# Performance work log

Measured on AMD Instinct MI355X. Metric: run time of the kernel, lower is better.

## Reference

```python
import jax, jax.numpy as jnp
import numpy as np

IMG_W, IMG_H = 640, 480
OS = 8            # roialign output_size
SCALE = 1.0       # spatial_scale (boxes already mapped to feature coords)
ALIGNED = True
ALPHA = 1.0       # student-t alpha


def _roi_align_one(feat, boxes):
    # feat: [C, H, W]; boxes: [sn, 4] (x1, y1, x2, y2) in feature coords.
    # torchvision RoIAlign, sampling_ratio=1 (one sample at each bin center).
    C, H, W = feat.shape
    off = 0.5 if ALIGNED else 0.0
    x1 = boxes[:, 0] * SCALE - off
    y1 = boxes[:, 1] * SCALE - off
    x2 = boxes[:, 2] * SCALE - off
    y2 = boxes[:, 3] * SCALE - off
    bw = (x2 - x1) / OS   # bin width  [sn]
    bh = (y2 - y1) / OS   # bin height [sn]
    grid = jnp.arange(OS, dtype=feat.dtype) + 0.5
    xs = x1[:, None] + grid * bw[:, None]   # [sn, OS]
    ys = y1[:, None] + grid * bh[:, None]   # [sn, OS]
    X = jnp.broadcast_to(xs[:, None, :], (xs.shape[0], OS, OS))  # [sn,OS,OS]
    Y = jnp.broadcast_to(ys[:, :, None], (ys.shape[0], OS, OS))
    valid = (Y >= -1.0) & (Y <= H) & (X >= -1.0) & (X <= W)
    y = jnp.clip(Y, 0.0, H - 1)
    x = jnp.clip(X, 0.0, W - 1)
    y0f = jnp.floor(y); x0f = jnp.floor(x)
    y0 = y0f.astype(jnp.int32); x0 = x0f.astype(jnp.int32)
    y1i = jnp.minimum(y0 + 1, H - 1); x1i = jnp.minimum(x0 + 1, W - 1)
    ly = y - y0f; lx = x - x0f
    hy = 1.0 - ly; hx = 1.0 - lx
    def g(yi, xi):
        return feat[:, yi, xi]  # [C, sn, OS, OS]
    val = (hy * hx)[None] * g(y0, x0) + (hy * lx)[None] * g(y0, x1i) \
        + (ly * hx)[None] * g(y1i, x0) + (ly * lx)[None] * g(y1i, x1i)
    val = jnp.where(valid[None], val, 0.0)
    return jnp.transpose(val, (1, 0, 2, 3))  # [sn, C, OS, OS]


def setup_inputs() -> dict:
    key = jax.random.key(0)
    ks = jax.random.split(key, 10)
    B, SN, C, T, FY, FX = 16, 64, 480, 2, 60, 80
    NDF1, NDF2, K = 1024, 256, 64
    z = jax.random.normal(ks[0], (B, C, T, FY, FX), jnp.float32)
    # boxes in image pixel coords
    cx = jax.random.uniform(ks[1], (B, SN), minval=0.1, maxval=0.9) * IMG_W
    cy = jax.random.uniform(ks[2], (B, SN), minval=0.1, maxval=0.9) * IMG_H
    bw = jax.random.uniform(ks[3], (B, SN), minval=0.05, maxval=0.3) * IMG_W
    bh = jax.random.uniform(ks[4], (B, SN), minval=0.05, maxval=0.3) * IMG_H
    x1 = jnp.clip(cx - bw / 2, 0.0, IMG_W); x2 = jnp.clip(cx + bw / 2, 0.0, IMG_W)
    y1 = jnp.clip(cy - bh / 2, 0.0, IMG_H); y2 = jnp.clip(cy + bh / 2, 0.0, IMG_H)
    bboxs = jnp.stack([x1, y1, x2, y2], axis=-1).astype(jnp.float32)
    din = C * OS * OS
    w1 = jax.random.normal(ks[5], (NDF1, din), jnp.float32) * (din ** -0.5)
    b1 = jnp.zeros((NDF1,), jnp.float32)
    w2 = jax.random.normal(ks[6], (NDF2, NDF1), jnp.float32) * (NDF1 ** -0.5)
    b2 = jnp.zeros((NDF2,), jnp.float32)
    centroids = jax.random.normal(ks[7], (K, NDF2), jnp.float32)
    return {"z": z, "bboxs": bboxs, "w1": w1, "b1": b1, "w2": w2, "b2": b2,
            "centroids": centroids}


def reference(z, bboxs, w1, b1, w2, b2, centroids):
    B, C, T, fy, fx = z.shape
    sn = bboxs.shape[1]
    # scale image-space boxes to feature coords (per (x,y) pair as in torch code)
    sc = jnp.array([fx / IMG_W, fy / IMG_H], jnp.float32)
    bb = (bboxs.reshape(B, sn, 2, 2) * sc).reshape(B, sn, 4)
    bb = jnp.nan_to_num(bb)
    feat = z[:, :, -1]  # [B, C, fy, fx]
    pooled = jax.vmap(_roi_align_one)(feat, bb)  # [B, sn, C, OS, OS]
    flat = pooled.reshape(B * sn, -1)
    e = flat @ w1.T + b1
    e = e @ w2.T + b2
    zz = e.reshape(B, sn, -1)  # [B, sn, ndf2]
    # student-t soft assignment (faithful: L2 norm, not squared)
    z2 = jnp.sum(zz * zz, axis=-1, keepdims=True)          # [B,sn,1]
    c2 = jnp.sum(centroids * centroids, axis=-1)           # [K]
    zc = jnp.einsum('bsd,kd->bsk', zz, centroids)          # [B,sn,K]
    nrm = jnp.sqrt(jnp.maximum(z2 + c2 - 2.0 * zc, 0.0))
    s = ((1.0 + nrm) / ALPHA) ** (-(ALPHA + 1.0) / 2.0)
    s = s / jnp.sum(s, axis=-1, keepdims=True)
    c = jnp.argmax(s, axis=2)
    return zz, s, c
```

## Files before the change

### kernel.cpp

```cpp
#include <hip/hip_runtime.h>
#include <hip/hip_bf16.h>

static constexpr int B_  = 16;
static constexpr int SN_ = 64;
static constexpr int C_  = 480;
static constexpr int T_  = 2;
static constexpr int FY_ = 60;
static constexpr int FX_ = 80;
static constexpr int OS_ = 8;
static constexpr int DIN = 30720;
static constexpr int M_  = 1024;
static constexpr int N1_ = 1024;
static constexpr int N2_ = 256;
static constexpr int K_  = 64;
static constexpr int SPLITK = 16;
static constexpr int NCH_ZZ = (DIN / 64) / SPLITK;
static constexpr int NCH_FW = N1_ / 32;
static constexpr int CPB = 2;
static constexpr int IMG = FY_ * FX_;
static constexpr int NB_W1T = (DIN / 64) * (N1_ / 64);
static constexpr int NB_W2P = N2_;
static constexpr int NB_FW  = 480;
static constexpr int NB_ROI = 16 * (C_ / CPB);

typedef __bf16 bf16x8 __attribute__((ext_vector_type(8)));
typedef float  f32x4  __attribute__((ext_vector_type(4)));
typedef unsigned int u32_as1 __attribute__((address_space(1)));
typedef unsigned int u32_as3 __attribute__((address_space(3)));

__device__ __forceinline__ float bf2f(unsigned short u) {
    union { unsigned int i; float f; } v; v.i = ((unsigned int)u) << 16; return v.f;
}
__device__ __forceinline__ unsigned short f2bf(float f) {
    unsigned int u = __float_as_uint(f);
    u = u + 0x7FFFu + ((u >> 16) & 1u);
    return (unsigned short)(u >> 16);
}
__device__ __forceinline__ void gll16(const void* g, void* l) {
    __builtin_amdgcn_global_load_lds((const u32_as1*)g, (u32_as3*)l, 16, 0, 0);
}

template<int NCHUNK, int SEG>
__device__ __forceinline__ void gemm_core(
    const unsigned short* __restrict__ Abase, long long Astride,
    const unsigned short* __restrict__ Bbase, long long Bstride,
    int k0, f32x4 (&acc)[4][2], unsigned short* L)
{
    const int t = threadIdx.x;
    const int w = t >> 6, lane = t & 63;
    const int rl8 = lane >> 3, slot = lane & 7;
    const int wm = w >> 2, wn = w & 3;
    const int fr = lane & 15, fg = lane >> 4;
    const int swz8 = (slot ^ rl8) * 8;

    long long arow[2], brow[2];
    int ci[2];
#pragma unroll
    for (int c = 0; c < 2; ++c) {
        ci[c] = w * 2 + c;
        const int row = ci[c] * 8 + rl8;
        arow[c] = (long long)row * Astride;
        brow[c] = (long long)row * Bstride;
    }

    auto stage = [&](int chunk, int par) {
        const int kin = k0 + chunk * 64;
        char* Lp = (char*)L + par * 65536;
#pragma unroll
        for (int c = 0; c < 2; ++c) {
            gll16(Abase + arow[c] + kin + swz8,       Lp + 0 * 16384 + ci[c] * 1024);
            gll16(Abase + arow[c] + SEG + kin + swz8, Lp + 1 * 16384 + ci[c] * 1024);
            gll16(Bbase + brow[c] + kin + swz8,       Lp + 2 * 16384 + ci[c] * 1024);
            gll16(Bbase + brow[c] + SEG + kin + swz8, Lp + 3 * 16384 + ci[c] * 1024);
        }
    };

    stage(0, 0);
    stage(1, 1);

    for (int it = 0; it < NCHUNK; ++it) {
        const int par = it & 1;
        if (it + 1 < NCHUNK) asm volatile("s_waitcnt vmcnt(8)" ::: "memory");
        else                 asm volatile("s_waitcnt vmcnt(0)" ::: "memory");
        __builtin_amdgcn_s_barrier();

        const char* Lp = (const char*)L + par * 65536;
        bf16x8 a[2][2][4], b[2][2][2];
#pragma unroll
        for (int hl = 0; hl < 2; ++hl)
#pragma unroll
            for (int ks = 0; ks < 2; ++ks)
#pragma unroll
                for (int mf = 0; mf < 4; ++mf) {
                    const int row = wm * 64 + mf * 16 + fr;
                    a[hl][ks][mf] = *reinterpret_cast<const bf16x8*>(
                        Lp + hl * 16384 + row * 128 + 16 * ((ks * 4 + fg) ^ (fr & 7)));
                }
#pragma unroll
        for (int hl = 0; hl < 2; ++hl)
#pragma unroll
            for (int ks = 0; ks < 2; ++ks)
#pragma unroll
                for (int nf = 0; nf < 2; ++nf) {
                    const int row = wn * 32 + nf * 16 + fr;
                    b[hl][ks][nf] = *reinterpret_cast<const bf16x8*>(
                        Lp + (2 + hl) * 16384 + row * 128 + 16 * ((ks * 4 + fg) ^ (fr & 7)));
                }
        asm volatile("s_waitcnt lgkmcnt(0)" ::: "memory");
        __builtin_amdgcn_sched_barrier(0);
        __builtin_amdgcn_s_barrier();
        __builtin_amdgcn_sched_barrier(0);
        if (it + 2 < NCHUNK) stage(it + 2, par);
        __builtin_amdgcn_sched_barrier(0);

        __builtin_amdgcn_s_setprio(1);
#pragma unroll
        for (int ks = 0; ks < 2; ++ks)
#pragma unroll
            for (int mf = 0; mf < 4; ++mf)
#pragma unroll
                for (int nf = 0; nf < 2; ++nf) {
                    acc[mf][nf] = __builtin_amdgcn_mfma_f32_16x16x32_bf16(
                        a[0][ks][mf], b[0][ks][nf], acc[mf][nf], 0, 0, 0);
                    acc[mf][nf] = __builtin_amdgcn_mfma_f32_16x16x32_bf16(
                        a[0][ks][mf], b[1][ks][nf], acc[mf][nf], 0, 0, 0);
                    acc[mf][nf] = __builtin_amdgcn_mfma_f32_16x16x32_bf16(
                        a[1][ks][mf], b[0][ks][nf], acc[mf][nf], 0, 0, 0);
                }
        __builtin_amdgcn_s_setprio(0);
    }
}

template<int NCHUNK, int SEG>
__device__ __forceinline__ void gemm_core32(
    const unsigned short* __restrict__ Abase, long long Astride,
    const unsigned short* __restrict__ Bbase, long long Bstride,
    int k0, f32x4 (&acc)[4][2], unsigned short* L)
{
    const int t = threadIdx.x;
    const int w = t >> 6, lane = t & 63;
    const int rl8 = lane >> 3, slot = lane & 7;
    const int wm = w >> 2, wn = w & 3;
    const int fr = lane & 15, fg = lane >> 4;
    const int g    = slot ^ rl8;
    const int goff = (g < 4) ? g * 8 : SEG + (g - 4) * 8;

    long long arow[2], brow[2];
    int ci[2];
#pragma unroll
    for (int c = 0; c < 2; ++c) {
        ci[c] = w * 2 + c;
        const int row = ci[c] * 8 + rl8;
        arow[c] = (long long)row * Astride;
        brow[c] = (long long)row * Bstride;
    }

    auto stage = [&](int chunk, int par) {
        const int kin = k0 + chunk * 32;
        char* Lp = (char*)L + par * 32768;
#pragma unroll
        for (int c = 0; c < 2; ++c) {
            gll16(Abase + arow[c] + goff + kin, Lp + 0 * 16384 + ci[c] * 1024);
            gll16(Bbase + brow[c] + goff + kin, Lp + 1 * 16384 + ci[c] * 1024);
        }
    };

    stage(0, 0);
    stage(1, 1);

    for (int it = 0; it < NCHUNK; ++it) {
        const int par = it & 1;
        if (it + 1 < NCHUNK) asm volatile("s_waitcnt vmcnt(4)" ::: "memory");
        else                 asm volatile("s_waitcnt vmcnt(0)" ::: "memory");
        __builtin_amdgcn_s_barrier();

        const char* Lp = (const char*)L + par * 32768;
        bf16x8 a[2][4], b[2][2];
#pragma unroll
        for (int hl = 0; hl < 2; ++hl)
#pragma unroll
            for (int mf = 0; mf < 4; ++mf) {
                const int row = wm * 64 + mf * 16 + fr;
                a[hl][mf] = *reinterpret_cast<const bf16x8*>(
                    Lp + row * 128 + 16 * ((hl * 4 + fg) ^ (fr & 7)));
            }
#pragma unroll
        for (int hl = 0; hl < 2; ++hl)
#pragma unroll
            for (int nf = 0; nf < 2; ++nf) {
                const int row = wn * 32 + nf * 16 + fr;
                b[hl][nf] = *reinterpret_cast<const bf16x8*>(
                    Lp + 16384 + row * 128 + 16 * ((hl * 4 + fg) ^ (fr & 7)));
            }
        asm volatile("s_waitcnt lgkmcnt(0)" ::: "memory");
        __builtin_amdgcn_sched_barrier(0);
        __builtin_amdgcn_s_barrier();
        __builtin_amdgcn_sched_barrier(0);
        if (it + 2 < NCHUNK) stage(it + 2, par);
        __builtin_amdgcn_sched_barrier(0);

        __builtin_amdgcn_s_setprio(1);
#pragma unroll
        for (int mf = 0; mf < 4; ++mf)
#pragma unroll
            for (int nf = 0; nf < 2; ++nf) {
                acc[mf][nf] = __builtin_amdgcn_mfma_f32_16x16x32_bf16(
                    a[0][mf], b[0][nf], acc[mf][nf], 0, 0, 0);
                acc[mf][nf] = __builtin_amdgcn_mfma_f32_16x16x32_bf16(
                    a[0][mf], b[1][nf], acc[mf][nf], 0, 0, 0);
                acc[mf][nf] = __builtin_amdgcn_mfma_f32_16x16x32_bf16(
                    a[1][mf], b[0][nf], acc[mf][nf], 0, 0, 0);
            }
        __builtin_amdgcn_s_setprio(0);
    }
}

__global__ __launch_bounds__(256) void prep1_kernel(
    const float* __restrict__ w1, const float* __restrict__ w2,
    const float* __restrict__ b1, const float* __restrict__ b2,
    unsigned short* __restrict__ w1T2, unsigned short* __restrict__ w2cat,
    float* __restrict__ bf) {
    __shared__ __align__(16) char smem[16640];
    const int blk = blockIdx.x;
    const int t = threadIdx.x;

    if (blk < NB_W1T) {
        float (*L)[65] = (float (*)[65])smem;
        const int q0 = (blk % (DIN / 64)) * 64, j0 = (blk / (DIN / 64)) * 64;
        const int tr = t >> 4, tc4 = (t & 15) * 4;
#pragma unroll
        for (int jj = 0; jj < 4; ++jj) {
            const int j = jj * 16 + tr;
            const float4 v = *(const float4*)(w1 + (size_t)(j0 + j) * DIN + q0 + tc4);
            L[j][tc4] = v.x; L[j][tc4 + 1] = v.y; L[j][tc4 + 2] = v.z; L[j][tc4 + 3] = v.w;
        }
        __syncthreads();
#pragma unroll
        for (int pass = 0; pass < 4; ++pass) {
            const int ql = pass * 16 + tr;
            const int jc = tc4;
            ushort4 h4, l4;
            float v0 = L[jc + 0][ql], v1 = L[jc + 1][ql], v2 = L[jc + 2][ql], v3 = L[jc + 3][ql];
            h4.x = f2bf(v0); l4.x = f2bf(v0 - bf2f(h4.x));
            h4.y = f2bf(v1); l4.y = f2bf(v1 - bf2f(h4.y));
            h4.z = f2bf(v2); l4.z = f2bf(v2 - bf2f(h4.z));
            h4.w = f2bf(v3); l4.w = f2bf(v3 - bf2f(h4.w));
            *(ushort4*)(w1T2 + (size_t)(q0 + ql) * 2048 + j0 + jc)        = h4;
            *(ushort4*)(w1T2 + (size_t)(q0 + ql) * 2048 + 1024 + j0 + jc) = l4;
        }
    } else {
        float* red = (float*)smem;
        const int p = blk - NB_W1T;
        float acc = 0.f;
#pragma unroll
        for (int j = t; j < N1_; j += 256) {
            const float v = w2[(size_t)p * N1_ + j];
            const unsigned short hi = f2bf(v);
            const unsigned short lo = f2bf(v - bf2f(hi));
            w2cat[(size_t)p * 2048 + j]        = hi;
            w2cat[(size_t)p * 2048 + 1024 + j] = lo;
            acc = fmaf(v, b1[j], acc);
        }
        red[t] = acc; __syncthreads();
        for (int s = 128; s > 0; s >>= 1) { if (t < s) red[t] += red[t + s]; __syncthreads(); }
        if (t == 0) bf[p] = red[0] + b2[p];
    }
}

__global__ __launch_bounds__(512, 4) void mega2_kernel(
    const float* __restrict__ z, const float* __restrict__ bboxs,
    const unsigned short* __restrict__ w2cat, const unsigned short* __restrict__ w1T2,
    unsigned short* __restrict__ W2, unsigned short* __restrict__ flat2) {
    __shared__ __align__(16) char smem[65536];
    const int blk = blockIdx.x;
    const int t = threadIdx.x;

    if (blk < NB_FW) {
        unsigned short* L = (unsigned short*)smem;
        const int xcd = blk & 7, j = blk >> 3;
        const int pb = j & 1;
        const int qb = xcd * 30 + (j >> 1);
        f32x4 acc[4][2];
#pragma unroll
        for (int i = 0; i < 4; ++i)
#pragma unroll
            for (int k = 0; k < 2; ++k) acc[i][k] = (f32x4){0.f, 0.f, 0.f, 0.f};

        gemm_core32<NCH_FW, N1_>(w2cat + (long long)pb * 128 * 2048, 2048,
                                 w1T2 + (long long)qb * 128 * 2048, 2048,
                                 0, acc, L);

        const int w = t >> 6, lane = t & 63;
        const int wm = w >> 2, wn = w & 3;
        const int fr = lane & 15, fg = lane >> 4;
#pragma unroll
        for (int mf = 0; mf < 4; ++mf)
#pragma unroll
            for (int nf = 0; nf < 2; ++nf)
#pragma unroll
                for (int r = 0; r < 4; ++r) {
                    const int p = pb * 128 + wm * 64 + mf * 16 + fg * 4 + r;
                    const int q = qb * 128 + wn * 32 + nf * 16 + fr;
                    const float v = acc[mf][nf][r];
                    const unsigned short hi = f2bf(v);
                    const unsigned short lo = f2bf(v - bf2f(hi));
                    W2[(size_t)p * (2 * DIN) + q]       = hi;
                    W2[(size_t)p * (2 * DIN) + DIN + q] = lo;
                }
    } else {
        float* img = (float*)smem;
        float (*bxc)[4] = (float (*)[4])(smem + 38400);
        const int idx = blk - NB_FW;
        const int b  = idx / (C_ / CPB);
        const int cg = idx % (C_ / CPB);
        const float* zb = z + ((size_t)b * C_ + (size_t)cg * CPB) * (size_t)(T_ * IMG)
                            + (size_t)(T_ - 1) * IMG;
#pragma unroll
        for (int c = 0; c < CPB; ++c) {
            const float4* src = (const float4*)(zb + (size_t)c * (T_ * IMG));
            float4* dst = (float4*)(img + c * IMG);
            for (int i = t; i < IMG / 4; i += 512) dst[i] = src[i];
        }
        if (t < 64) {
            const float* bp = bboxs + ((size_t)b * 64 + t) * 4;
            const float v0 = bp[0], v1 = bp[1], v2 = bp[2], v3 = bp[3];
            bxc[t][0] = isnan(v0) ? 0.f : v0;
            bxc[t][1] = isnan(v1) ? 0.f : v1;
            bxc[t][2] = isnan(v2) ? 0.f : v2;
            bxc[t][3] = isnan(v3) ? 0.f : v3;
        }
        __syncthreads();

        const int p = t & 63, mh = t >> 6;
        const int gy = p >> 3, gx = p & 7;
        for (int mq = 0; mq < 8; ++mq) {
            const int m = mq * 8 + mh;
            const float x1 = bxc[m][0] * 0.125f - 0.5f;
            const float y1 = bxc[m][1] * 0.125f - 0.5f;
            const float x2 = bxc[m][2] * 0.125f - 0.5f;
            const float y2 = bxc[m][3] * 0.125f - 0.5f;
            const float bw = (x2 - x1) * (1.0f / OS_);
            const float bh = (y2 - y1) * (1.0f / OS_);
            const float X = x1 + ((float)gx + 0.5f) * bw;
            const float Y = y1 + ((float)gy + 0.5f) * bh;
            const bool valid = (Y >= -1.0f) && (Y <= (float)FY_) &&
                               (X >= -1.0f) && (X <= (float)FX_);
            const float yc = fminf(fmaxf(Y, 0.f), (float)(FY_ - 1));
            const float xc = fminf(fmaxf(X, 0.f), (float)(FX_ - 1));
            const float y0f = floorf(yc), x0f = floorf(xc);
            const int y0 = (int)y0f, x0 = (int)x0f;
            const int y1i = min(y0 + 1, FY_ - 1);
            const int x1i = min(x0 + 1, FX_ - 1);
            const float ly = yc - y0f, lx = xc - x0f;
            const float hy = 1.f - ly,  hx = 1.f - lx;
            float w00 = hy * hx, w01 = hy * lx, w10 = ly * hx, w11 = ly * lx;
            if (!valid) { w00 = 0.f; w01 = 0.f; w10 = 0.f; w11 = 0.f; }
            const int i00 = y0 * FX_ + x0, i01 = y0 * FX_ + x1i;
            const int i10 = y1i * FX_ + x0, i11 = y1i * FX_ + x1i;
            unsigned short* fo = flat2 + (size_t)(b * 64 + m) * (2 * DIN)
                                       + cg * (CPB * 64) + p;
#pragma unroll
            for (int c = 0; c < CPB; ++c) {
                const float* f = img + c * IMG;
                const float v = w00 * f[i00] + w01 * f[i01] + w10 * f[i10] + w11 * f[i11];
                const unsigned short hi = f2bf(v);
                const unsigned short lo = f2bf(v - bf2f(hi));
                fo[c * 64]       = hi;
                fo[DIN + c * 64] = lo;
            }
        }
    }
}

__global__ __launch_bounds__(512, 1) void zz_mfma(const unsigned short* __restrict__ flat2,
                                                  const unsigned short* __restrict__ W2,
                                                  float* __restrict__ part) {
    __shared__ __align__(16) unsigned short L[2 * 4 * 128 * 64];
    const int bid = blockIdx.x;
    const int xcd = bid & 7, j = bid >> 3;
    const int mb = j & 7;
    const int pair = xcd * 4 + (j >> 3);
    const int nb = pair & 1, sp = pair >> 1;
    f32x4 acc[4][2];
#pragma unroll
    for (int i = 0; i < 4; ++i)
#pragma unroll
        for (int k = 0; k < 2; ++k) acc[i][k] = (f32x4){0.f, 0.f, 0.f, 0.f};

    gemm_core<NCH_ZZ, DIN>(flat2 + (long long)mb * 128 * (2 * DIN), 2 * DIN,
                           W2 + (long long)nb * 128 * (2 * DIN), 2 * DIN,
                           sp * (NCH_ZZ * 64), acc, L);

    float* po = part + (size_t)sp * (M_ * N2_);
    const int t = threadIdx.x;
    const int w = t >> 6, lane = t & 63;
    const int wm = w >> 2, wn = w & 3;
    const int fr = lane & 15, fg = lane >> 4;
#pragma unroll
    for (int mf = 0; mf < 4; ++mf)
#pragma unroll
        for (int nf = 0; nf < 2; ++nf)
#pragma unroll
            for (int r = 0; r < 4; ++r) {
                const int m = mb * 128 + wm * 64 + mf * 16 + fg * 4 + r;
                const int n = nb * 128 + wn * 32 + nf * 16 + fr;
                po[(size_t)m * N2_ + n] = acc[mf][nf][r];
            }
}

__global__ __launch_bounds__(256) void reduce_cluster_kernel(
    const float* __restrict__ part, const float* __restrict__ bf,
    const float* __restrict__ cent,
    float* __restrict__ out_zz, float* __restrict__ out_s, float* __restrict__ out_c) {
    __shared__ float row[N2_];
    const int m = blockIdx.x, t = threadIdx.x;
    float a = bf[t];
#pragma unroll
    for (int s = 0; s < SPLITK; ++s) a += part[(size_t)s * (M_ * N2_) + (size_t)m * N2_ + t];
    out_zz[(size_t)m * N2_ + t] = a;
    row[t] = a;
    __syncthreads();
    if (t < 64) {
        const float* cr = cent + (size_t)t * N2_;
        float dot = 0.f, c2 = 0.f, z2 = 0.f;
        for (int d = 0; d < N2_; ++d) {
            const float zv = row[d], cv = cr[d];
            dot = fmaf(zv, cv, dot);
            c2  = fmaf(cv, cv, c2);
            z2  = fmaf(zv, zv, z2);
        }
        const float nrm = sqrtf(fmaxf(z2 + c2 - 2.f * dot, 0.f));
        const float su = 1.0f / (1.0f + nrm);
        float ssum = su;
#pragma unroll
        for (int mk = 1; mk < 64; mk <<= 1) ssum += __shfl_xor(ssum, mk, 64);
        const float s = su / ssum;
        out_s[(size_t)m * 64 + t] = s;
        float bv = s; int bi = t;
#pragma unroll
        for (int mk = 1; mk < 64; mk <<= 1) {
            const float ov = __shfl_xor(bv, mk, 64);
            const int   oi = __shfl_xor(bi, mk, 64);
            if (ov > bv || (ov == bv && oi < bi)) { bv = ov; bi = oi; }
        }
        if (t == 0) out_c[m] = (float)bi;
    }
}

extern "C" void kernel_launch(void* const* d_in, const int* in_sizes, int n_in,
                              void* d_out, int out_size, void* d_ws, size_t ws_size,
                              hipStream_t stream) {
    const float* z     = (const float*)d_in[0];
    const float* bboxs = (const float*)d_in[1];
    const float* w1    = (const float*)d_in[2];
    const float* b1    = (const float*)d_in[3];
    const float* w2    = (const float*)d_in[4];
    const float* b2    = (const float*)d_in[5];
    const float* cent  = (const float*)d_in[6];
    float* out = (float*)d_out;
    float* out_zz = out;
    float* out_s  = out + (size_t)M_ * N2_;
    float* out_c  = out + (size_t)M_ * N2_ + (size_t)M_ * K_;

    char* ws = (char*)d_ws;
    unsigned short* w1T2   = (unsigned short*)(ws);
    unsigned short* flat2  = (unsigned short*)(ws + 125829120u);
    unsigned short* W2     = (unsigned short*)(ws + 251658240u);
    float*          part   = (float*)(ws + 283115520u);
    unsigned short* w2cat  = (unsigned short*)(ws + 316669952u);
    float*          bfused = (float*)(ws + 317718528u);

    prep1_kernel<<<dim3(NB_W1T + NB_W2P), dim3(256), 0, stream>>>(
        w1, w2, b1, b2, w1T2, w2cat, bfused);
    mega2_kernel<<<dim3(NB_FW + NB_ROI), dim3(512), 0, stream>>>(
        z, bboxs, w2cat, w1T2, W2, flat2);
    zz_mfma<<<dim3(256), dim3(512), 0, stream>>>(flat2, W2, part);
    reduce_cluster_kernel<<<dim3(1024), dim3(256), 0, stream>>>(part, bfused, cent,
                                                                out_zz, out_s, out_c);
}
```

Before: 228.4 us.

## Move RoIAlign pooling into prep kernel and give weight-fusion GEMM its own kernel

```diff
diff --git a/kernel.cpp b/kernel.cpp
--- a/kernel.cpp
+++ b/kernel.cpp
@@ -18,10 +18,9 @@
 static constexpr int NCH_FW = N1_ / 32;
 static constexpr int CPB = 2;
 static constexpr int IMG = FY_ * FX_;
+static constexpr int NB_ROI = 16 * (C_ / CPB);
 static constexpr int NB_W1T = (DIN / 64) * (N1_ / 64);
 static constexpr int NB_W2P = N2_;
-static constexpr int NB_FW  = 480;
-static constexpr int NB_ROI = 16 * (C_ / CPB);
 
 typedef __bf16 bf16x8 __attribute__((ext_vector_type(8)));
 typedef float  f32x4  __attribute__((ext_vector_type(4)));
@@ -215,111 +214,28 @@
     }
 }
 
-__global__ __launch_bounds__(256) void prep1_kernel(
+__global__ __launch_bounds__(256) void prep_kernel(
+    const float* __restrict__ z, const float* __restrict__ bboxs,
     const float* __restrict__ w1, const float* __restrict__ w2,
     const float* __restrict__ b1, const float* __restrict__ b2,
-    unsigned short* __restrict__ w1T2, unsigned short* __restrict__ w2cat,
-    float* __restrict__ bf) {
-    __shared__ __align__(16) char smem[16640];
+    unsigned short* __restrict__ flat2, unsigned short* __restrict__ w1T2,
+    unsigned short* __restrict__ w2cat, float* __restrict__ bf) {
+    __shared__ __align__(16) char smem[39424];
     const int blk = blockIdx.x;
     const int t = threadIdx.x;
 
-    if (blk < NB_W1T) {
-        float (*L)[65] = (float (*)[65])smem;
-        const int q0 = (blk % (DIN / 64)) * 64, j0 = (blk / (DIN / 64)) * 64;
-        const int tr = t >> 4, tc4 = (t & 15) * 4;
-#pragma unroll
-        for (int jj = 0; jj < 4; ++jj) {
-            const int j = jj * 16 + tr;
-            const float4 v = *(const float4*)(w1 + (size_t)(j0 + j) * DIN + q0 + tc4);
-            L[j][tc4] = v.x; L[j][tc4 + 1] = v.y; L[j][tc4 + 2] = v.z; L[j][tc4 + 3] = v.w;
-        }
-        __syncthreads();
-#pragma unroll
-        for (int pass = 0; pass < 4; ++pass) {
-            const int ql = pass * 16 + tr;
-            const int jc = tc4;
-            ushort4 h4, l4;
-            float v0 = L[jc + 0][ql], v1 = L[jc + 1][ql], v2 = L[jc + 2][ql], v3 = L[jc + 3][ql];
-            h4.x = f2bf(v0); l4.x = f2bf(v0 - bf2f(h4.x));
-            h4.y = f2bf(v1); l4.y = f2bf(v1 - bf2f(h4.y));
-            h4.z = f2bf(v2); l4.z = f2bf(v2 - bf2f(h4.z));
-            h4.w = f2bf(v3); l4.w = f2bf(v3 - bf2f(h4.w));
-            *(ushort4*)(w1T2 + (size_t)(q0 + ql) * 2048 + j0 + jc)        = h4;
-            *(ushort4*)(w1T2 + (size_t)(q0 + ql) * 2048 + 1024 + j0 + jc) = l4;
-        }
-    } else {
-        float* red = (float*)smem;
-        const int p = blk - NB_W1T;
-        float acc = 0.f;
-#pragma unroll
-        for (int j = t; j < N1_; j += 256) {
-            const float v = w2[(size_t)p * N1_ + j];
-            const unsigned short hi = f2bf(v);
-            const unsigned short lo = f2bf(v - bf2f(hi));
-            w2cat[(size_t)p * 2048 + j]        = hi;
-            w2cat[(size_t)p * 2048 + 1024 + j] = lo;
-            acc = fmaf(v, b1[j], acc);
-        }
-        red[t] = acc; __syncthreads();
-        for (int s = 128; s > 0; s >>= 1) { if (t < s) red[t] += red[t + s]; __syncthreads(); }
-        if (t == 0) bf[p] = red[0] + b2[p];
-    }
-}
-
-__global__ __launch_bounds__(512, 4) void mega2_kernel(
-    const float* __restrict__ z, const float* __restrict__ bboxs,
-    const unsigned short* __restrict__ w2cat, const unsigned short* __restrict__ w1T2,
-    unsigned short* __restrict__ W2, unsigned short* __restrict__ flat2) {
-    __shared__ __align__(16) char smem[65536];
-    const int blk = blockIdx.x;
-    const int t = threadIdx.x;
-
-    if (blk < NB_FW) {
-        unsigned short* L = (unsigned short*)smem;
-        const int xcd = blk & 7, j = blk >> 3;
-        const int pb = j & 1;
-        const int qb = xcd * 30 + (j >> 1);
-        f32x4 acc[4][2];
-#pragma unroll
-        for (int i = 0; i < 4; ++i)
-#pragma unroll
-            for (int k = 0; k < 2; ++k) acc[i][k] = (f32x4){0.f, 0.f, 0.f, 0.f};
-
-        gemm_core32<NCH_FW, N1_>(w2cat + (long long)pb * 128 * 2048, 2048,
-                                 w1T2 + (long long)qb * 128 * 2048, 2048,
-                                 0, acc, L);
-
-        const int w = t >> 6, lane = t & 63;
-        const int wm = w >> 2, wn = w & 3;
-        const int fr = lane & 15, fg = lane >> 4;
-#pragma unroll
-        for (int mf = 0; mf < 4; ++mf)
-#pragma unroll
-            for (int nf = 0; nf < 2; ++nf)
-#pragma unroll
-                for (int r = 0; r < 4; ++r) {
-                    const int p = pb * 128 + wm * 64 + mf * 16 + fg * 4 + r;
-                    const int q = qb * 128 + wn * 32 + nf * 16 + fr;
-                    const float v = acc[mf][nf][r];
-                    const unsigned short hi = f2bf(v);
-                    const unsigned short lo = f2bf(v - bf2f(hi));
-                    W2[(size_t)p * (2 * DIN) + q]       = hi;
-                    W2[(size_t)p * (2 * DIN) + DIN + q] = lo;
-                }
-    } else {
+    if (blk < NB_ROI) {
         float* img = (float*)smem;
         float (*bxc)[4] = (float (*)[4])(smem + 38400);
-        const int idx = blk - NB_FW;
-        const int b  = idx / (C_ / CPB);
-        const int cg = idx % (C_ / CPB);
+        const int b  = blk / (C_ / CPB);
+        const int cg = blk % (C_ / CPB);
         const float* zb = z + ((size_t)b * C_ + (size_t)cg * CPB) * (size_t)(T_ * IMG)
                             + (size_t)(T_ - 1) * IMG;
 #pragma unroll
         for (int c = 0; c < CPB; ++c) {
             const float4* src = (const float4*)(zb + (size_t)c * (T_ * IMG));
             float4* dst = (float4*)(img + c * IMG);
-            for (int i = t; i < IMG / 4; i += 512) dst[i] = src[i];
+            for (int i = t; i < IMG / 4; i += 256) dst[i] = src[i];
         }
         if (t < 64) {
             const float* bp = bboxs + ((size_t)b * 64 + t) * 4;
@@ -333,8 +249,8 @@
 
         const int p = t & 63, mh = t >> 6;
         const int gy = p >> 3, gx = p & 7;
-        for (int mq = 0; mq < 8; ++mq) {
-            const int m = mq * 8 + mh;
+        for (int mq = 0; mq < 16; ++mq) {
+            const int m = mq * 4 + mh;
             const float x1 = bxc[m][0] * 0.125f - 0.5f;
             const float y1 = bxc[m][1] * 0.125f - 0.5f;
             const float x2 = bxc[m][2] * 0.125f - 0.5f;
@@ -369,7 +285,86 @@
                 fo[DIN + c * 64] = lo;
             }
         }
-    }
+    } else if (blk < NB_ROI + NB_W1T) {
+        float (*L)[65] = (float (*)[65])smem;
+        const int idx = blk - NB_ROI;
+        const int q0 = (idx % (DIN / 64)) * 64, j0 = (idx / (DIN / 64)) * 64;
+        const int tr = t >> 4, tc4 = (t & 15) * 4;
+#pragma unroll
+        for (int jj = 0; jj < 4; ++jj) {
+            const int j = jj * 16 + tr;
+            const float4 v = *(const float4*)(w1 + (size_t)(j0 + j) * DIN + q0 + tc4);
+            L[j][tc4] = v.x; L[j][tc4 + 1] = v.y; L[j][tc4 + 2] = v.z; L[j][tc4 + 3] = v.w;
+        }
+        __syncthreads();
+#pragma unroll
+        for (int pass = 0; pass < 4; ++pass) {
+            const int ql = pass * 16 + tr;
+            const int jc = tc4;
+            ushort4 h4, l4;
+            float v0 = L[jc + 0][ql], v1 = L[jc + 1][ql], v2 = L[jc + 2][ql], v3 = L[jc + 3][ql];
+            h4.x = f2bf(v0); l4.x = f2bf(v0 - bf2f(h4.x));
+            h4.y = f2bf(v1); l4.y = f2bf(v1 - bf2f(h4.y));
+            h4.z = f2bf(v2); l4.z = f2bf(v2 - bf2f(h4.z));
+            h4.w = f2bf(v3); l4.w = f2bf(v3 - bf2f(h4.w));
+            *(ushort4*)(w1T2 + (size_t)(q0 + ql) * 2048 + j0 + jc)        = h4;
+            *(ushort4*)(w1T2 + (size_t)(q0 + ql) * 2048 + 1024 + j0 + jc) = l4;
+        }
+    } else {
+        float* red = (float*)smem;
+        const int p = blk - (NB_ROI + NB_W1T);
+        float acc = 0.f;
+#pragma unroll
+        for (int j = t; j < N1_; j += 256) {
+            const float v = w2[(size_t)p * N1_ + j];
+            const unsigned short hi = f2bf(v);
+            const unsigned short lo = f2bf(v - bf2f(hi));
+            w2cat[(size_t)p * 2048 + j]        = hi;
+            w2cat[(size_t)p * 2048 + 1024 + j] = lo;
+            acc = fmaf(v, b1[j], acc);
+        }
+        red[t] = acc; __syncthreads();
+        for (int s = 128; s > 0; s >>= 1) { if (t < s) red[t] += red[t + s]; __syncthreads(); }
+        if (t == 0) bf[p] = red[0] + b2[p];
+    }
+}
+
+__global__ __launch_bounds__(512, 2) void fusew_mfma(const unsigned short* __restrict__ w2cat,
+                                                     const unsigned short* __restrict__ w1T2,
+                                                     unsigned short* __restrict__ W2) {
+    __shared__ __align__(16) unsigned short L[2 * 2 * 128 * 64];
+    const int bid = blockIdx.x;
+    const int xcd = bid & 7, j = bid >> 3;
+    const int pb = j & 1;
+    const int qb = xcd * 30 + (j >> 1);
+    f32x4 acc[4][2];
+#pragma unroll
+    for (int i = 0; i < 4; ++i)
+#pragma unroll
+        for (int k = 0; k < 2; ++k) acc[i][k] = (f32x4){0.f, 0.f, 0.f, 0.f};
+
+    gemm_core32<NCH_FW, N1_>(w2cat + (long long)pb * 128 * 2048, 2048,
+                             w1T2 + (long long)qb * 128 * 2048, 2048,
+                             0, acc, L);
+
+    const int t = threadIdx.x;
+    const int w = t >> 6, lane = t & 63;
+    const int wm = w >> 2, wn = w & 3;
+    const int fr = lane & 15, fg = lane >> 4;
+#pragma unroll
+    for (int mf = 0; mf < 4; ++mf)
+#pragma unroll
+        for (int nf = 0; nf < 2; ++nf)
+#pragma unroll
+            for (int r = 0; r < 4; ++r) {
+                const int p = pb * 128 + wm * 64 + mf * 16 + fg * 4 + r;
+                const int q = qb * 128 + wn * 32 + nf * 16 + fr;
+                const float v = acc[mf][nf][r];
+                const unsigned short hi = f2bf(v);
+                const unsigned short lo = f2bf(v - bf2f(hi));
+                W2[(size_t)p * (2 * DIN) + q]       = hi;
+                W2[(size_t)p * (2 * DIN) + DIN + q] = lo;
+            }
 }
 
 __global__ __launch_bounds__(512, 1) void zz_mfma(const unsigned short* __restrict__ flat2,
@@ -470,10 +465,9 @@
     unsigned short* w2cat  = (unsigned short*)(ws + 316669952u);
     float*          bfused = (float*)(ws + 317718528u);
 
-    prep1_kernel<<<dim3(NB_W1T + NB_W2P), dim3(256), 0, stream>>>(
-        w1, w2, b1, b2, w1T2, w2cat, bfused);
-    mega2_kernel<<<dim3(NB_FW + NB_ROI), dim3(512), 0, stream>>>(
-        z, bboxs, w2cat, w1T2, W2, flat2);
+    prep_kernel<<<dim3(NB_ROI + NB_W1T + NB_W2P), dim3(256), 0, stream>>>(
+        z, bboxs, w1, w2, b1, b2, flat2, w1T2, w2cat, bfused);
+    fusew_mfma<<<dim3(480), dim3(512), 0, stream>>>(w2cat, w1T2, W2);
     zz_mfma<<<dim3(256), dim3(512), 0, stream>>>(flat2, W2, part);
     reduce_cluster_kernel<<<dim3(1024), dim3(256), 0, stream>>>(part, bfused, cent,
                                                                 out_zz, out_s, out_c);
```

Result: no change. 226.7 us (-0.7%).
